# Kernel tuning notes

Measured on AMD Instinct MI355X. Metric: run time of the kernel, lower is better.

The kernel has to match this reference:

```python
import jax, jax.numpy as jnp
import numpy as np

NUM_HEADS = 16

def setup_inputs() -> dict:
    key = jax.random.key(0)
    k1, k2, k3 = jax.random.split(key, 3)
    B, T, C = 2, 2048, 1024
    x = jax.random.normal(k1, (B, T, C), dtype=jnp.float32)
    w_qkv = jax.random.normal(k2, (3 * C, C), dtype=jnp.float32) * (C ** -0.5)
    w_out = jax.random.normal(k3, (C, C), dtype=jnp.float32) * (C ** -0.5)
    b_out = jnp.zeros((C,), dtype=jnp.float32)
    return {"x": x, "w_qkv": w_qkv, "w_out": w_out, "b_out": b_out}

def reference(x, w_qkv, w_out, b_out):
    B, T, C = x.shape
    H = NUM_HEADS
    dh = C // H
    scale = 1.0 / jnp.sqrt(jnp.float32(dh))
    # fused qkv projection (torch Linear: x @ W^T), no bias
    qkv = jnp.einsum('btc,dc->btd', x, w_qkv)  # [B,T,3C]
    q, k, v = jnp.split(qkv, 3, axis=-1)
    # [B,H,T,dh]
    q = q.reshape(B, T, H, dh).transpose(0, 2, 1, 3)
    k = k.reshape(B, T, H, dh).transpose(0, 2, 1, 3)
    v = v.reshape(B, T, H, dh).transpose(0, 2, 1, 3)
    att = jnp.einsum('bhqd,bhkd->bhqk', q, k) * scale  # [B,H,T,T]
    causal = jnp.tril(jnp.ones((T, T), dtype=bool))
    att = jnp.where(causal[None, None, :, :], att, jnp.float32(-jnp.inf))
    att = jax.nn.softmax(att, axis=-1)
    y = jnp.einsum('bhqk,bhkd->bhqd', att, v)  # [B,H,T,dh]
    y = y.transpose(0, 2, 1, 3).reshape(B, T, C)
    y = jnp.einsum('btc,dc->btd', y, w_out) + b_out
    return y
```

## Files before the change

### kernel.cpp

```cpp
#include <hip/hip_runtime.h>
#include <hip/hip_bf16.h>
#include <math.h>

typedef __bf16 bf16x8 __attribute__((ext_vector_type(8)));
typedef __bf16 bf16x4 __attribute__((ext_vector_type(4)));
typedef float  f32x4  __attribute__((ext_vector_type(4)));

#define MFMA16(A, B, C) __builtin_amdgcn_mfma_f32_16x16x32_bf16(A, B, C, 0, 0, 0)

__device__ __forceinline__ void gload_lds16(const void* g, void* l) {
  __builtin_amdgcn_global_load_lds((const __attribute__((address_space(1))) void*)g,
                                   (__attribute__((address_space(3))) void*)l, 16, 0, 0);
}

__device__ __forceinline__ float exp2_fast(float x) {
  float r; asm("v_exp_f32 %0, %1" : "=v"(r) : "v"(x)); return r;
}

__device__ __forceinline__ unsigned lds_off(const void* p) {
  return (unsigned)(size_t)(const __attribute__((address_space(3))) void*)p;
}

__device__ __forceinline__ bf16x4 ds_tr16(unsigned byte_addr) {
  bf16x4 r;
  asm volatile("ds_read_b64_tr_b16 %0, %1" : "=v"(r) : "v"(byte_addr));
  return r;
}

__global__ __launch_bounds__(256) void cvt_f32_bf16(const float* __restrict__ src,
                                                    __bf16* __restrict__ dst, int n) {
  const int i = (blockIdx.x * 256 + threadIdx.x) * 8;
  if (i >= n) return;
  const float4 a = *(const float4*)(src + i);
  const float4 b = *(const float4*)(src + i + 4);
  bf16x8 v;
  v[0] = (__bf16)a.x; v[1] = (__bf16)a.y; v[2] = (__bf16)a.z; v[3] = (__bf16)a.w;
  v[4] = (__bf16)b.x; v[5] = (__bf16)b.y; v[6] = (__bf16)b.z; v[7] = (__bf16)b.w;
  *(bf16x8*)(dst + i) = v;
}

template <bool BIAS, typename CT>
__global__ __launch_bounds__(256) void gemm_bt(const __bf16* __restrict__ A,
                                               const __bf16* __restrict__ B,
                                               const float* __restrict__ bias,
                                               CT* __restrict__ C, int M, int N, int K) {
  __shared__ alignas(16) __bf16 As[2][128 * 32];
  __shared__ alignas(16) __bf16 Bs[2][128 * 32];

  const int tid  = threadIdx.x;
  const int lane = tid & 63;
  const int wv   = tid >> 6;
  const int wr   = wv >> 1, wc = wv & 1;
  const int row0 = blockIdx.y * 128;
  const int col0 = blockIdx.x * 128;
  const int NT   = K >> 5;

  f32x4 acc[4][4] = {};

  auto stage = [&](int buf, int kt) {
    const int k0 = kt << 5;
#pragma unroll
    for (int i = 0; i < 2; ++i) {
      const int n    = i * 256 + tid;
      const int row  = n >> 2;
      const int slot = (n & 3) ^ ((row >> 1) & 3);
      gload_lds16(A + (size_t)(row0 + row) * K + (k0 + slot * 8),
                  &As[buf][(i * 256 + wv * 64) * 8]);
    }
#pragma unroll
    for (int i = 0; i < 2; ++i) {
      const int n    = i * 256 + tid;
      const int row  = n >> 2;
      const int slot = (n & 3) ^ ((row >> 1) & 3);
      gload_lds16(B + (size_t)(col0 + row) * K + (k0 + slot * 8),
                  &Bs[buf][(i * 256 + wv * 64) * 8]);
    }
  };

  stage(0, 0);
  __syncthreads();
  int cur = 0;
  for (int kt = 0; kt < NT; ++kt) {
    if (kt + 1 < NT) stage(cur ^ 1, kt + 1);

    bf16x8 af[4], bfr[4];
#pragma unroll
    for (int m = 0; m < 4; ++m) {
      const int row  = wr * 64 + m * 16 + (lane & 15);
      const int slot = (lane >> 4) ^ ((row >> 1) & 3);
      af[m] = *(const bf16x8*)&As[cur][row * 32 + slot * 8];
    }
#pragma unroll
    for (int n = 0; n < 4; ++n) {
      const int row  = wc * 64 + n * 16 + (lane & 15);
      const int slot = (lane >> 4) ^ ((row >> 1) & 3);
      bfr[n] = *(const bf16x8*)&Bs[cur][row * 32 + slot * 8];
    }
#pragma unroll
    for (int m = 0; m < 4; ++m)
#pragma unroll
      for (int n = 0; n < 4; ++n) acc[m][n] = MFMA16(af[m], bfr[n], acc[m][n]);

    __syncthreads();
    cur ^= 1;
  }

#pragma unroll
  for (int n = 0; n < 4; ++n) {
    const int   col = col0 + wc * 64 + n * 16 + (lane & 15);
    const float bv  = BIAS ? bias[col] : 0.0f;
#pragma unroll
    for (int m = 0; m < 4; ++m) {
      const int rbase = row0 + wr * 64 + m * 16 + ((lane >> 4) << 2);
#pragma unroll
      for (int r = 0; r < 4; ++r)
        C[(size_t)(rbase + r) * N + col] = (CT)(acc[m][n][r] + bv);
    }
  }
}

__global__ __launch_bounds__(256) void attn_fwd(const __bf16* __restrict__ qkv,
                                                __bf16* __restrict__ yo) {
  __shared__ alignas(16) __bf16 Ks[2][64 * 64];
  __shared__ alignas(16) __bf16 Vs[2][64 * 64];

  const int tid  = threadIdx.x;
  const int lane = tid & 63;
  const int ql   = lane & 15;
  const int g    = lane >> 4;
  const int wv   = tid >> 6;

  const int bid = blockIdx.x;
  const int qt  = 31 - (bid >> 5);
  const int bh  = bid & 31;
  const int b   = bh >> 4;
  const int h   = bh & 15;
  const int q0  = qt * 64;
  const int qw  = q0 + wv * 16;
  const int NT  = qt + 1;

  const size_t  rs = 3072;
  const __bf16* Qg = qkv + (size_t)b * 2048 * rs + h * 64;
  const __bf16* Kg = Qg + 1024;
  const __bf16* Vg = Qg + 2048;

  auto stageK = [&](int buf, int t) {
#pragma unroll
    for (int i = 0; i < 2; ++i) {
      const int n = i * 256 + tid, row = n >> 3, slot = (n & 7) ^ (row & 7);
      gload_lds16(Kg + (size_t)((t << 6) + row) * rs + slot * 8,
                  &Ks[buf][(i * 256 + wv * 64) * 8]);
    }
  };
  auto stageV = [&](int buf, int t) {
#pragma unroll
    for (int i = 0; i < 2; ++i) {
      const int n   = i * 256 + tid;
      const int key = ((n >> 5) << 2) + ((n >> 1) & 3);
      const int d   = (((n >> 3) & 3) << 4) + ((n & 1) << 3);
      gload_lds16(Vg + (size_t)((t << 6) + key) * rs + d, &Vs[buf][(i * 256 + wv * 64) * 8]);
    }
  };

  bf16x8 aQ[2];
#pragma unroll
  for (int ks = 0; ks < 2; ++ks)
    aQ[ks] = *(const bf16x8*)(Qg + (size_t)(qw + ql) * rs + ks * 32 + (g << 3));

  bf16x8 vones;
#pragma unroll
  for (int e = 0; e < 8; ++e) vones[e] = (__bf16)1.0f;

  f32x4 o[5] = {};
  float m2 = -INFINITY;

  const float SCALE2 = 0.125f * 1.44269504088896f;
  const float THR    = 8.0f;
  const unsigned vbase = lds_off(&Vs[0][0]);

  const int bidx0 = ((lane & 16) << 3) + (ql << 2);
  const int bidx1 = bidx0 + 64;

  int cur = 0;
  stageK(0, 0);
  stageV(0, 0);
  __syncthreads();

  for (int t = 0; t < NT; ++t) {
    const int  k0  = t << 6;
    const bool pre = (t + 1 < NT);
    if (pre) { stageK(cur ^ 1, t + 1); stageV(cur ^ 1, t + 1); }

    f32x4 sc[4] = {};
    __builtin_amdgcn_s_setprio(1);
#pragma unroll
    for (int n = 0; n < 4; ++n) {
#pragma unroll
      for (int ks = 0; ks < 2; ++ks) {
        const int krow = n * 16 + ql;
        const int slot = ((ks << 2) + g) ^ (krow & 7);
        bf16x8    kf   = *(const bf16x8*)&Ks[cur][krow * 64 + slot * 8];
        sc[n]          = MFMA16(kf, aQ[ks], sc[n]);
      }
    }
    __builtin_amdgcn_s_setprio(0);

    const unsigned abase = vbase + (cur ? 8192u : 0u) + (g << 10) + (ql << 3);
    bf16x4 vlo[2][4], vhi[2][4];
#pragma unroll
    for (int ks = 0; ks < 2; ++ks)
#pragma unroll
      for (int n = 0; n < 4; ++n) {
        vlo[ks][n] = ds_tr16(abase + ks * 4096 + n * 128);
        vhi[ks][n] = ds_tr16(abase + ks * 4096 + n * 128 + 512);
      }

    float s16[4][4];
    float mx = -INFINITY;
    if (t == NT - 1) {
      const int q = qw + ql;
#pragma unroll
      for (int n = 0; n < 4; ++n)
#pragma unroll
        for (int r = 0; r < 4; ++r) {
          const int k = k0 + n * 16 + (g << 2) + r;
          float     s = sc[n][r] * SCALE2;
          if (k > q) s = -INFINITY;
          s16[n][r] = s;
          mx        = fmaxf(mx, s);
        }
    } else {
#pragma unroll
      for (int n = 0; n < 4; ++n)
#pragma unroll
        for (int r = 0; r < 4; ++r) {
          const float s = sc[n][r] * SCALE2;
          s16[n][r]     = s;
          mx            = fmaxf(mx, s);
        }
    }
    mx = fmaxf(mx, __shfl_xor(mx, 16, 64));
    mx = fmaxf(mx, __shfl_xor(mx, 32, 64));

    if (__any(mx - m2 > THR)) {
      const float mnew = fmaxf(m2, mx);
      const float lsc  = exp2_fast(m2 - mnew);
      m2               = mnew;
      float lf[4];
#pragma unroll
      for (int r = 0; r < 4; ++r)
        lf[r] = __int_as_float(__builtin_amdgcn_ds_bpermute(
            ((g << 2) + r) << 2, __float_as_int(lsc)));
#pragma unroll
      for (int n = 0; n < 5; ++n)
#pragma unroll
        for (int r = 0; r < 4; ++r) o[n][r] *= lf[r];
    }

    int W[8];
#pragma unroll
    for (int n = 0; n < 4; ++n)
#pragma unroll
      for (int rp = 0; rp < 2; ++rp) {
        union { __bf16 h[2]; int i; } pk;
        pk.h[0]      = (__bf16)exp2_fast(s16[n][2 * rp] - m2);
        pk.h[1]      = (__bf16)exp2_fast(s16[n][2 * rp + 1] - m2);
        W[2 * n + rp] = pk.i;
      }

    union { int w[4]; bf16x8 v; } pa[2];
#pragma unroll
    for (int ks = 0; ks < 2; ++ks)
#pragma unroll
      for (int w = 0; w < 4; ++w) {
        const int idx = (w < 2) ? bidx0 : bidx1;
        const int t0  = __builtin_amdgcn_ds_bpermute(idx, W[4 * ks + (w & 1)]);
        const int t1  = __builtin_amdgcn_ds_bpermute(idx, W[4 * ks + 2 + (w & 1)]);
        pa[ks].w[w]   = (lane & 32) ? t1 : t0;
      }

    asm volatile("s_waitcnt lgkmcnt(0)");
    __builtin_amdgcn_sched_barrier(0);

    __builtin_amdgcn_s_setprio(1);
#pragma unroll
    for (int ks = 0; ks < 2; ++ks) {
#pragma unroll
      for (int n = 0; n < 4; ++n) {
        bf16x8 vf;
#pragma unroll
        for (int e = 0; e < 4; ++e) { vf[e] = vlo[ks][n][e]; vf[e + 4] = vhi[ks][n][e]; }
        o[n] = MFMA16(pa[ks].v, vf, o[n]);
      }
      o[4] = MFMA16(pa[ks].v, vones, o[4]);
    }
    __builtin_amdgcn_s_setprio(0);

    __syncthreads();
    cur ^= 1;
  }

#pragma unroll
  for (int n = 0; n < 4; ++n) {
    const int d = n * 16 + ql;
#pragma unroll
    for (int r = 0; r < 4; ++r) {
      const int q = qw + (g << 2) + r;
      yo[((size_t)b * 2048 + q) * 1024 + h * 64 + d] = (__bf16)(o[n][r] / o[4][r]);
    }
  }
}

extern "C" void kernel_launch(void* const* d_in, const int* in_sizes, int n_in, void* d_out,
                              int out_size, void* d_ws, size_t ws_size, hipStream_t stream) {
  (void)in_sizes; (void)n_in; (void)out_size; (void)ws_size;
  const float* x     = (const float*)d_in[0];
  const float* w_qkv = (const float*)d_in[1];
  const float* w_out = (const float*)d_in[2];
  const float* b_out = (const float*)d_in[3];
  float*       out   = (float*)d_out;

  __bf16* xb    = (__bf16*)d_ws;
  __bf16* wqkvb = xb + (size_t)4096 * 1024;
  __bf16* woutb = wqkvb + (size_t)3072 * 1024;
  __bf16* qkv   = woutb + (size_t)1024 * 1024;
  __bf16* yatt  = qkv + (size_t)4096 * 3072;

  cvt_f32_bf16<<<(4096 * 1024) / (256 * 8), 256, 0, stream>>>(x, xb, 4096 * 1024);
  cvt_f32_bf16<<<(3072 * 1024) / (256 * 8), 256, 0, stream>>>(w_qkv, wqkvb, 3072 * 1024);
  cvt_f32_bf16<<<(1024 * 1024) / (256 * 8), 256, 0, stream>>>(w_out, woutb, 1024 * 1024);

  gemm_bt<false, __bf16><<<dim3(24, 32), 256, 0, stream>>>(xb, wqkvb, nullptr, qkv,
                                                           4096, 3072, 1024);
  attn_fwd<<<1024, 256, 0, stream>>>(qkv, yatt);
  gemm_bt<true, float><<<dim3(8, 32), 256, 0, stream>>>(yatt, woutb, b_out, out,
                                                        4096, 1024, 1024);
}
```

Before: 119.4 us.

## Merge conversion kernels, precompute staging pointers, fold softmax scale into Q

Replaces the three f32-to-bf16 conversion launches with a single kernel that dispatches on the element index, removing two launches. In the attention kernel, the K/V staging addresses are computed once and advanced by a fixed stride instead of recomputed each tile. The 1/8 softmax scale is folded into Q in bf16, and log2(e) moves into an FMA inside the exponent, with the rescale threshold adjusted to match. Scaling Q by 0.125 in bf16 is exact (power of two), so accuracy risk is small.

```diff
diff --git a/kernel.cpp b/kernel.cpp
--- a/kernel.cpp
+++ b/kernel.cpp
@@ -27,16 +27,28 @@
   return r;
 }
 
-__global__ __launch_bounds__(256) void cvt_f32_bf16(const float* __restrict__ src,
-                                                    __bf16* __restrict__ dst, int n) {
-  const int i = (blockIdx.x * 256 + threadIdx.x) * 8;
-  if (i >= n) return;
-  const float4 a = *(const float4*)(src + i);
-  const float4 b = *(const float4*)(src + i + 4);
+__global__ __launch_bounds__(256) void cvt_all(const float* __restrict__ x,
+                                               const float* __restrict__ wq,
+                                               const float* __restrict__ wo,
+                                               __bf16* __restrict__ xb,
+                                               __bf16* __restrict__ wqb,
+                                               __bf16* __restrict__ wob) {
+  int i = (blockIdx.x * 256 + threadIdx.x) * 8;
+  const float* s;
+  __bf16*      d;
+  if (i < 4194304) {
+    s = x; d = xb;
+  } else if (i < 4194304 + 3145728) {
+    i -= 4194304; s = wq; d = wqb;
+  } else {
+    i -= 4194304 + 3145728; s = wo; d = wob;
+  }
+  const float4 a = *(const float4*)(s + i);
+  const float4 b = *(const float4*)(s + i + 4);
   bf16x8 v;
   v[0] = (__bf16)a.x; v[1] = (__bf16)a.y; v[2] = (__bf16)a.z; v[3] = (__bf16)a.w;
   v[4] = (__bf16)b.x; v[5] = (__bf16)b.y; v[6] = (__bf16)b.z; v[7] = (__bf16)b.w;
-  *(bf16x8*)(dst + i) = v;
+  *(bf16x8*)(d + i) = v;
 }
 
 template <bool BIAS, typename CT>
@@ -144,28 +156,30 @@
   const __bf16* Kg = Qg + 1024;
   const __bf16* Vg = Qg + 2048;
 
-  auto stageK = [&](int buf, int t) {
-#pragma unroll
-    for (int i = 0; i < 2; ++i) {
-      const int n = i * 256 + tid, row = n >> 3, slot = (n & 7) ^ (row & 7);
-      gload_lds16(Kg + (size_t)((t << 6) + row) * rs + slot * 8,
-                  &Ks[buf][(i * 256 + wv * 64) * 8]);
-    }
+  const int slotK = ((tid & 7) ^ ((tid >> 3) & 7)) << 3;
+  const int keyV  = ((tid >> 5) << 2) + ((tid >> 1) & 3);
+  const int dV    = (((tid >> 3) & 3) << 4) + ((tid & 1) << 3);
+  const __bf16* kP0 = Kg + (size_t)(tid >> 3) * rs + slotK;
+  const __bf16* kP1 = kP0 + 32 * rs;
+  const __bf16* vP0 = Vg + (size_t)keyV * rs + dV;
+  const __bf16* vP1 = vP0 + 32 * rs;
+  const size_t  step = 64 * rs;
+
+  auto stageKV = [&](int buf) {
+    gload_lds16(kP0, &Ks[buf][wv * 512]);
+    gload_lds16(kP1, &Ks[buf][2048 + wv * 512]);
+    gload_lds16(vP0, &Vs[buf][wv * 512]);
+    gload_lds16(vP1, &Vs[buf][2048 + wv * 512]);
+    kP0 += step; kP1 += step; vP0 += step; vP1 += step;
   };
-  auto stageV = [&](int buf, int t) {
-#pragma unroll
-    for (int i = 0; i < 2; ++i) {
-      const int n   = i * 256 + tid;
-      const int key = ((n >> 5) << 2) + ((n >> 1) & 3);
-      const int d   = (((n >> 3) & 3) << 4) + ((n & 1) << 3);
-      gload_lds16(Vg + (size_t)((t << 6) + key) * rs + d, &Vs[buf][(i * 256 + wv * 64) * 8]);
-    }
-  };
 
   bf16x8 aQ[2];
 #pragma unroll
-  for (int ks = 0; ks < 2; ++ks)
+  for (int ks = 0; ks < 2; ++ks) {
     aQ[ks] = *(const bf16x8*)(Qg + (size_t)(qw + ql) * rs + ks * 32 + (g << 3));
+#pragma unroll
+    for (int e = 0; e < 8; ++e) aQ[ks][e] = aQ[ks][e] * (__bf16)0.125f;
+  }
 
   bf16x8 vones;
 #pragma unroll
@@ -174,22 +188,21 @@
   f32x4 o[5] = {};
   float m2 = -INFINITY;
 
-  const float SCALE2 = 0.125f * 1.44269504088896f;
-  const float THR    = 8.0f;
+  const float L   = 1.44269504088896f;
+  const float THR = 5.5451774f;
   const unsigned vbase = lds_off(&Vs[0][0]);
 
   const int bidx0 = ((lane & 16) << 3) + (ql << 2);
   const int bidx1 = bidx0 + 64;
 
   int cur = 0;
-  stageK(0, 0);
-  stageV(0, 0);
+  stageKV(0);
   __syncthreads();
 
   for (int t = 0; t < NT; ++t) {
     const int  k0  = t << 6;
     const bool pre = (t + 1 < NT);
-    if (pre) { stageK(cur ^ 1, t + 1); stageV(cur ^ 1, t + 1); }
+    if (pre) stageKV(cur ^ 1);
 
     f32x4 sc[4] = {};
     __builtin_amdgcn_s_setprio(1);
@@ -224,7 +237,7 @@
 #pragma unroll
         for (int r = 0; r < 4; ++r) {
           const int k = k0 + n * 16 + (g << 2) + r;
-          float     s = sc[n][r] * SCALE2;
+          float     s = sc[n][r];
           if (k > q) s = -INFINITY;
           s16[n][r] = s;
           mx        = fmaxf(mx, s);
@@ -234,7 +247,7 @@
       for (int n = 0; n < 4; ++n)
 #pragma unroll
         for (int r = 0; r < 4; ++r) {
-          const float s = sc[n][r] * SCALE2;
+          const float s = sc[n][r];
           s16[n][r]     = s;
           mx            = fmaxf(mx, s);
         }
@@ -244,7 +257,7 @@
 
     if (__any(mx - m2 > THR)) {
       const float mnew = fmaxf(m2, mx);
-      const float lsc  = exp2_fast(m2 - mnew);
+      const float lsc  = exp2_fast((m2 - mnew) * L);
       m2               = mnew;
       float lf[4];
 #pragma unroll
@@ -257,14 +270,15 @@
         for (int r = 0; r < 4; ++r) o[n][r] *= lf[r];
     }
 
+    const float mL = m2 * L;
     int W[8];
 #pragma unroll
     for (int n = 0; n < 4; ++n)
 #pragma unroll
       for (int rp = 0; rp < 2; ++rp) {
         union { __bf16 h[2]; int i; } pk;
-        pk.h[0]      = (__bf16)exp2_fast(s16[n][2 * rp] - m2);
-        pk.h[1]      = (__bf16)exp2_fast(s16[n][2 * rp + 1] - m2);
+        pk.h[0]      = (__bf16)exp2_fast(__builtin_fmaf(s16[n][2 * rp], L, -mL));
+        pk.h[1]      = (__bf16)exp2_fast(__builtin_fmaf(s16[n][2 * rp + 1], L, -mL));
         W[2 * n + rp] = pk.i;
       }
 
@@ -326,9 +340,7 @@
   __bf16* qkv   = woutb + (size_t)1024 * 1024;
   __bf16* yatt  = qkv + (size_t)4096 * 3072;
 
-  cvt_f32_bf16<<<(4096 * 1024) / (256 * 8), 256, 0, stream>>>(x, xb, 4096 * 1024);
-  cvt_f32_bf16<<<(3072 * 1024) / (256 * 8), 256, 0, stream>>>(w_qkv, wqkvb, 3072 * 1024);
-  cvt_f32_bf16<<<(1024 * 1024) / (256 * 8), 256, 0, stream>>>(w_out, woutb, 1024 * 1024);
+  cvt_all<<<4096, 256, 0, stream>>>(x, w_qkv, w_out, xb, wqkvb, woutb);
 
   gemm_bt<false, __bf16><<<dim3(24, 32), 256, 0, stream>>>(xb, wqkvb, nullptr, qkv,
                                                            4096, 3072, 1024);
```

After: 113.2 us. 1.05x faster.
